# Kernel optimization log

Measured on AMD Instinct MI355X. Metric: run time of the kernel, lower is better.

## Reference

```python
import jax, jax.numpy as jnp
import numpy as np

DIM = 512
INNER = 512        # heads(8) * dim_head(64)
OUT_DIM = 256
SCALE = 64 ** -0.5  # dim_head ** -0.5
BN_EPS = 1e-5


def setup_inputs() -> dict:
    key = jax.random.key(0)
    ks = jax.random.split(key, 8)
    B, H, W = 2, 96, 320
    return {
        "left_feat": jax.random.normal(ks[0], (B, DIM, H, W), jnp.float32),
        "right_feat": jax.random.normal(ks[1], (B, DIM, H, W), jnp.float32),
        "wq": jax.random.normal(ks[2], (INNER, DIM), jnp.float32) * (DIM ** -0.5),
        "wk": jax.random.normal(ks[3], (INNER, DIM), jnp.float32) * (DIM ** -0.5),
        "wv": jax.random.normal(ks[4], (INNER, DIM), jnp.float32) * (DIM ** -0.5),
        "w1": jax.random.normal(ks[5], (OUT_DIM, INNER * 2), jnp.float32) * ((INNER * 2) ** -0.5),
        "bn_gamma": jnp.ones((OUT_DIM,), jnp.float32),
        "bn_beta": jnp.zeros((OUT_DIM,), jnp.float32),
        "bn_mean": jnp.zeros((OUT_DIM,), jnp.float32),
        "bn_var": jnp.ones((OUT_DIM,), jnp.float32),
        "w2": jax.random.normal(ks[6], (OUT_DIM, OUT_DIM), jnp.float32) * (OUT_DIM ** -0.5),
    }


def reference(left_feat, right_feat, wq, wk, wv, w1, bn_gamma, bn_beta, bn_mean, bn_var, w2):
    # conv1x1 projections, directly producing channels-last [b, h, w, c]
    q = jnp.einsum('bchw,oc->bhwo', left_feat, wq)
    k = jnp.einsum('bchw,oc->bhwo', right_feat, wk)
    v = jnp.einsum('bchw,oc->bhwo', right_feat, wv)
    # cross-attention along width, independently per (batch, row)
    dots = jnp.einsum('bhwc,bhxc->bhwx', q, k) * SCALE   # [b, h, w, w]
    attn = jax.nn.softmax(dots, axis=-1)
    out = jnp.einsum('bhwx,bhxc->bhwc', attn, v)         # [b, h, w, c]
    out = out.transpose(0, 3, 1, 2)                      # [b, c, h, w]
    new_left = jnp.concatenate([left_feat, out], axis=1)  # [b, 2*inner, h, w]
    # to_out: conv1x1 -> BN (eval mode, running stats) -> LeakyReLU(0.2) -> conv1x1
    y = jnp.einsum('bchw,oc->bohw', new_left, w1)
    inv = jax.lax.rsqrt(bn_var + BN_EPS)
    y = (y - bn_mean[None, :, None, None]) * (inv * bn_gamma)[None, :, None, None] \
        + bn_beta[None, :, None, None]
    y = jnp.where(y >= 0, y, 0.2 * y)
    return jnp.einsum('bchw,oc->bohw', y, w2)
```

## Files before the change

### kernel.cpp

```cpp
#include <hip/hip_runtime.h>

typedef __bf16 bf16x8 __attribute__((ext_vector_type(8)));
typedef float f32x4 __attribute__((ext_vector_type(4)));
typedef unsigned short u16x8 __attribute__((ext_vector_type(8)));
typedef unsigned short u16x4 __attribute__((ext_vector_type(4)));

#define MFMA16(a, b, c) __builtin_amdgcn_mfma_f32_16x16x32_bf16((a), (b), (c), 0, 0, 0)
#define GLOAD_LDS(gp, lp) __builtin_amdgcn_global_load_lds( \
    (const __attribute__((address_space(1))) void*)(uintptr_t)(const void*)(gp), \
    (__attribute__((address_space(3))) void*)(uintptr_t)(void*)(lp), 16, 0, 0)

#define NB 2
#define NC 512
#define NH 96
#define NW 320
#define PH 30720
#define NPIX 61440
#define NOUT 256

__device__ __forceinline__ unsigned short f2bf(float f) {
    union { float f; unsigned u; } v; v.f = f;
    unsigned r = v.u + 0x7fffu + ((v.u >> 16) & 1u);
    return (unsigned short)(r >> 16);
}

__global__ void k_cast(const float* __restrict__ src, unsigned short* __restrict__ dst, int n) {
    int i = blockIdx.x * 256 + threadIdx.x;
    if (i < n) dst[i] = f2bf(src[i]);
}

__global__ __launch_bounds__(256) void k_wtrans(
        const float* __restrict__ wq, const float* __restrict__ wk, const float* __restrict__ wv,
        unsigned short* __restrict__ WqT, unsigned short* __restrict__ WkT, unsigned short* __restrict__ WvT) {
    __shared__ float t[64][65];
    int z = blockIdx.z;
    const float* src = (z == 0) ? wq : (z == 1) ? wk : wv;
    unsigned short* dst = (z == 0) ? WqT : (z == 1) ? WkT : WvT;
    int i0 = blockIdx.y * 64;
    int c0 = blockIdx.x * 64;
    int tt = threadIdx.x;
    int r4 = tt >> 4, px = (tt & 15) * 4;
#pragma unroll
    for (int i = 0; i < 4; ++i) {
        int il = i * 16 + r4;
        f32x4 v = *reinterpret_cast<const f32x4*>(src + (size_t)(i0 + il) * 512 + c0 + px);
        t[il][px + 0] = v[0]; t[il][px + 1] = v[1]; t[il][px + 2] = v[2]; t[il][px + 3] = v[3];
    }
    __syncthreads();
    int cc = (tt & 7) * 8, pl0 = tt >> 3;
#pragma unroll
    for (int j = 0; j < 2; ++j) {
        int pl = j * 32 + pl0;
        u16x8 ov;
#pragma unroll
        for (int i = 0; i < 8; ++i) ov[i] = f2bf(t[cc + i][pl]);
        *reinterpret_cast<u16x8*>(dst + (size_t)(c0 + pl) * 512 + i0 + cc) = ov;
    }
}

__global__ __launch_bounds__(256) void k_transpose(
        const float* __restrict__ L, const float* __restrict__ R,
        unsigned short* __restrict__ Lcl, unsigned short* __restrict__ Rcl,
        unsigned short* __restrict__ Rbf) {
    __shared__ float t[64][65];
    int z = blockIdx.z;
    int b = z & 1, which = z >> 1;
    const float* src = which ? R : L;
    unsigned short* dst = which ? Rcl : Lcl;
    int c0 = blockIdx.y * 64;
    int p0 = blockIdx.x * 64;
    int tt = threadIdx.x;

    int cl4 = tt >> 4;
    int px = (tt & 15) * 4;
#pragma unroll
    for (int i = 0; i < 4; ++i) {
        int cl = i * 16 + cl4;
        f32x4 v = *reinterpret_cast<const f32x4*>(src + (size_t)(b * NC + c0 + cl) * PH + p0 + px);
        t[cl][px + 0] = v[0];
        t[cl][px + 1] = v[1];
        t[cl][px + 2] = v[2];
        t[cl][px + 3] = v[3];
        if (which) {
            u16x4 sv;
#pragma unroll
            for (int k = 0; k < 4; ++k) sv[k] = f2bf(v[k]);
            *reinterpret_cast<u16x4*>(Rbf + (size_t)(b * NC + c0 + cl) * PH + p0 + px) = sv;
        }
    }
    __syncthreads();

    int cc = (tt & 7) * 8;
    int pl0 = tt >> 3;
#pragma unroll
    for (int j = 0; j < 2; ++j) {
        int pl = j * 32 + pl0;
        u16x8 ov;
#pragma unroll
        for (int i = 0; i < 8; ++i) ov[i] = f2bf(t[cc + i][pl]);
        *reinterpret_cast<u16x8*>(dst + (size_t)(b * PH + p0 + pl) * NC + c0 + cc) = ov;
    }
}

template <int MODE>
__global__ __launch_bounds__(256) void k_gemm(
        const unsigned short* __restrict__ A0,
        const unsigned short* __restrict__ A1,
        const unsigned short* __restrict__ Bb,
        const unsigned short* __restrict__ Bb2,
        unsigned short* __restrict__ Dbf,
        float* __restrict__ Df32,
        const float* __restrict__ g, const float* __restrict__ be,
        const float* __restrict__ mu, const float* __restrict__ va) {
    constexpr int SA = (MODE == 4) ? NOUT : (MODE == 6) ? 1024 : NC;
    constexpr int AOFF = (MODE == 6) ? 512 : 0;
    constexpr int SB = (MODE == 3) ? 1024 : (MODE == 4) ? NOUT : NC;
    constexpr int KS = (MODE == 3) ? 32 : (MODE == 4) ? 8 : 16;
    constexpr int NTO = (MODE == 3 || MODE == 4) ? 2 : 4;
    constexpr int TOT = (MODE == 5) ? 16 : (MODE == 6) ? 8 : ((MODE == 3 || MODE == 4) ? 960 : 1920);

    __shared__ unsigned short Asm[2][128 * 32];
    __shared__ unsigned short Bsm[2][128 * 32];

    int pphys = blockIdx.x;
    int lgc = (pphys & 7) * (TOT / 8) + (pphys >> 3);
    int pixt = lgc / NTO, ot = lgc % NTO;
    const int mbase = ((MODE == 4) ? ot : pixt) * 128;
    const int nbase = ((MODE == 4) ? pixt : ot) * 128;

    const int lane = threadIdx.x & 63, w = threadIdx.x >> 6;
    const int lr = lane & 15, lg = lane >> 4;
    const int wr = w >> 1, wc = w & 1;

    auto stageA = [&](int buf, int kc) {
        const unsigned short* srcA = A0;
        int colOff = kc * 32;
        if constexpr (MODE == 3) {
            if (kc >= 16) { srcA = A1; colOff = (kc - 16) * 32; }
        }
#pragma unroll
        for (int j = 0; j < 2; ++j) {
            int cb = w * 128 + j * 64;
            int c = cb + lane;
            const unsigned short* gp = srcA + (size_t)(mbase + (c >> 2)) * SA + AOFF + colOff + (c & 3) * 8;
            GLOAD_LDS(gp, Asm[buf] + cb * 8);
        }
    };
    auto stageB = [&](int buf, int kc) {
        const unsigned short* srcB = Bb;
        int colOff = kc * 32;
        int sb = SB;
        if constexpr (MODE == 3) {
            if (kc >= 16) { srcB = Bb2; colOff = (kc - 16) * 32; sb = 512; }
        }
#pragma unroll
        for (int j = 0; j < 2; ++j) {
            int cb = w * 128 + j * 64;
            int c = cb + lane;
            const unsigned short* gp = srcB + (size_t)(nbase + (c >> 2)) * sb + colOff + (c & 3) * 8;
            GLOAD_LDS(gp, Bsm[buf] + cb * 8);
        }
    };

    f32x4 acc[4][4] = {};

    stageA(0, 0);
    stageB(0, 0);
    __syncthreads();

    for (int kc = 0; kc < KS; ++kc) {
        int cur = kc & 1;
        if (kc + 1 < KS) {
            stageA(cur ^ 1, kc + 1);
            stageB(cur ^ 1, kc + 1);
        }
        bf16x8 af[4], bfr[4];
#pragma unroll
        for (int i = 0; i < 4; ++i)
            af[i] = *reinterpret_cast<const bf16x8*>(Asm[cur] + (wr * 64 + i * 16 + lr) * 32 + lg * 8);
#pragma unroll
        for (int j = 0; j < 4; ++j)
            bfr[j] = *reinterpret_cast<const bf16x8*>(Bsm[cur] + (wc * 64 + j * 16 + lr) * 32 + lg * 8);
        __builtin_amdgcn_s_setprio(1);
#pragma unroll
        for (int i = 0; i < 4; ++i)
#pragma unroll
            for (int j = 0; j < 4; ++j)
                acc[i][j] = MFMA16(af[i], bfr[j], acc[i][j]);
        __builtin_amdgcn_s_setprio(0);
        __syncthreads();
    }

    const int lr4 = lg * 4;
    if constexpr (MODE == 0 || MODE >= 5) {
#pragma unroll
        for (int i = 0; i < 4; ++i)
#pragma unroll
            for (int j = 0; j < 4; ++j) {
                int ocol = nbase + wc * 64 + j * 16 + lr;
#pragma unroll
                for (int r = 0; r < 4; ++r) {
                    int prow = mbase + wr * 64 + i * 16 + lr4 + r;
                    Dbf[(size_t)prow * NC + ocol] = f2bf(acc[i][j][r]);
                }
            }
    } else if constexpr (MODE == 3) {
#pragma unroll
        for (int j = 0; j < 4; ++j) {
            int o = nbase + wc * 64 + j * 16 + lr;
            float sc = g[o] * rsqrtf(va[o] + 1e-5f);
            float sh = be[o] - mu[o] * sc;
#pragma unroll
            for (int i = 0; i < 4; ++i)
#pragma unroll
                for (int r = 0; r < 4; ++r) {
                    int prow = mbase + wr * 64 + i * 16 + lr4 + r;
                    float y = acc[i][j][r] * sc + sh;
                    y = (y >= 0.f) ? y : 0.2f * y;
                    Dbf[(size_t)prow * NOUT + o] = f2bf(y);
                }
        }
    } else {
#pragma unroll
        for (int j = 0; j < 4; ++j) {
            int pix = nbase + wc * 64 + j * 16 + lr;
            int b = pix / PH, ph = pix % PH;
#pragma unroll
            for (int i = 0; i < 4; ++i)
#pragma unroll
                for (int r = 0; r < 4; ++r) {
                    int o = mbase + wr * 64 + i * 16 + lr4 + r;
                    Df32[((size_t)b * NOUT + o) * PH + ph] = acc[i][j][r];
                }
        }
    }
}

__global__ __launch_bounds__(256, 2) void k_attn(
        const unsigned short* __restrict__ Q, const unsigned short* __restrict__ K,
        const unsigned short* __restrict__ Vb, unsigned short* __restrict__ O) {
    __shared__ unsigned short P[64][328];
    __shared__ unsigned short KV[32 * 512];

    int pphys = blockIdx.x;
    int l = (pphys & 7) * 120 + (pphys >> 3);
    int head = l / 5, qt = l % 5;
    int b = head / NH, hh = head % NH;
    int lane = threadIdx.x & 63, w = threadIdx.x >> 6;
    int lr = lane & 15, lg = lane >> 4;
    int rowbase = b * PH + hh * NW;
    int qrow = rowbase + qt * 64 + w * 16 + lr;

    bf16x8 qf[16];
#pragma unroll
    for (int kc = 0; kc < 16; ++kc)
        qf[kc] = *reinterpret_cast<const bf16x8*>(Q + (size_t)qrow * NC + kc * 32 + lg * 8);

    f32x4 acc[20];
#pragma unroll
    for (int xt = 0; xt < 20; ++xt) acc[xt] = f32x4{0.f, 0.f, 0.f, 0.f};

    u16x8 kreg[4];
    auto kload = [&](int t) {
#pragma unroll
        for (int j = 0; j < 4; ++j) {
            int r = w * 4 + j;
            kreg[j] = *reinterpret_cast<const u16x8*>(
                K + (size_t)(rowbase + t * 16 + r) * NC + ((lane ^ (r & 7)) * 8));
        }
    };
    auto kwrite = [&](int buf) {
#pragma unroll
        for (int j = 0; j < 4; ++j) {
            int r = w * 4 + j;
            *reinterpret_cast<u16x8*>(KV + (buf * 16 + r) * 512 + lane * 8) = kreg[j];
        }
    };

    kload(0);
    kwrite(0);
    __syncthreads();
#pragma unroll
    for (int t = 0; t < 20; ++t) {
        if (t + 1 < 20) kload(t + 1);
        int buf = t & 1;
        int rsw = lr & 7;
        __builtin_amdgcn_s_setprio(1);
#pragma unroll
        for (int kc = 0; kc < 16; ++kc) {
            bf16x8 kf = *reinterpret_cast<const bf16x8*>(
                KV + (buf * 16 + lr) * 512 + (((kc * 4 + lg) ^ rsw) * 8));
            acc[t] = MFMA16(qf[kc], kf, acc[t]);
        }
        __builtin_amdgcn_s_setprio(0);
        __syncthreads();
        if (t + 1 < 20) kwrite(buf ^ 1);
        __syncthreads();
    }

    u16x8 vreg[8];
    auto vload = [&](int s) {
#pragma unroll
        for (int j = 0; j < 8; ++j) {
            int c = (w * 8 + j) * 16 + (lane >> 2);
            int qg = (lane & 3) ^ ((lane >> 3) & 3);
            vreg[j] = *reinterpret_cast<const u16x8*>(
                Vb + (size_t)(b * NC + c) * PH + hh * NW + s * 32 + qg * 8);
        }
    };
    auto vwrite = [&]() {
#pragma unroll
        for (int j = 0; j < 8; ++j)
            *reinterpret_cast<u16x8*>(KV + (w * 8 + j) * 512 + lane * 8) = vreg[j];
    };
    vload(0);

#pragma unroll
    for (int xt = 0; xt < 20; ++xt)
#pragma unroll
        for (int r = 0; r < 4; ++r) acc[xt][r] *= 0.125f;
    float m[4] = {-1e30f, -1e30f, -1e30f, -1e30f};
#pragma unroll
    for (int xt = 0; xt < 20; ++xt)
#pragma unroll
        for (int r = 0; r < 4; ++r) m[r] = fmaxf(m[r], acc[xt][r]);
#pragma unroll
    for (int mask = 1; mask < 16; mask <<= 1)
#pragma unroll
        for (int r = 0; r < 4; ++r) m[r] = fmaxf(m[r], __shfl_xor(m[r], mask));
    float s4[4] = {0.f, 0.f, 0.f, 0.f};
#pragma unroll
    for (int xt = 0; xt < 20; ++xt)
#pragma unroll
        for (int r = 0; r < 4; ++r) {
            float e = __expf(acc[xt][r] - m[r]);
            acc[xt][r] = e;
            s4[r] += e;
        }
#pragma unroll
    for (int mask = 1; mask < 16; mask <<= 1)
#pragma unroll
        for (int r = 0; r < 4; ++r) s4[r] += __shfl_xor(s4[r], mask);
#pragma unroll
    for (int xt = 0; xt < 20; ++xt)
#pragma unroll
        for (int r = 0; r < 4; ++r)
            P[w * 16 + lg * 4 + r][xt * 16 + lr] = f2bf(acc[xt][r]);
    __syncthreads();
    vwrite();
    __syncthreads();

    f32x4 oacc[32];
#pragma unroll
    for (int ct = 0; ct < 32; ++ct) oacc[ct] = f32x4{0.f, 0.f, 0.f, 0.f};

#pragma unroll
    for (int s = 0; s < 10; ++s) {
        if (s + 1 < 10) vload(s + 1);
        bf16x8 pf = *reinterpret_cast<const bf16x8*>(&P[w * 16 + lr][s * 32 + lg * 8]);
        __builtin_amdgcn_s_setprio(1);
#pragma unroll
        for (int ct = 0; ct < 32; ++ct) {
            bf16x8 vf = *reinterpret_cast<const bf16x8*>(
                KV + ct * 512 + lr * 32 + ((lg ^ ((lr >> 1) & 3)) * 8));
            oacc[ct] = MFMA16(pf, vf, oacc[ct]);
        }
        __builtin_amdgcn_s_setprio(0);
        __syncthreads();
        if (s + 1 < 10) vwrite();
        __syncthreads();
    }

#pragma unroll
    for (int ct = 0; ct < 32; ++ct)
#pragma unroll
        for (int r = 0; r < 4; ++r) {
            int prow = rowbase + qt * 64 + w * 16 + lg * 4 + r;
            O[(size_t)prow * NC + ct * 16 + lr] = f2bf(oacc[ct][r] / s4[r]);
        }
}

extern "C" void kernel_launch(void* const* d_in, const int* in_sizes, int n_in,
                              void* d_out, int out_size, void* d_ws, size_t ws_size,
                              hipStream_t stream) {
    const float* left  = (const float*)d_in[0];
    const float* right = (const float*)d_in[1];
    const float* wq = (const float*)d_in[2];
    const float* wk = (const float*)d_in[3];
    const float* wv = (const float*)d_in[4];
    const float* w1 = (const float*)d_in[5];
    const float* bn_g = (const float*)d_in[6];
    const float* bn_b = (const float*)d_in[7];
    const float* bn_m = (const float*)d_in[8];
    const float* bn_v = (const float*)d_in[9];
    const float* w2 = (const float*)d_in[10];
    float* out = (float*)d_out;

    size_t off = 0;
    auto alloc = [&](size_t bytes) -> void* {
        void* p = (char*)d_ws + off;
        off += (bytes + 255) & ~(size_t)255;
        return p;
    };
    const size_t clb = (size_t)NPIX * NC * 2;
    unsigned short* Lcl = (unsigned short*)alloc(clb);
    unsigned short* Rcl = (unsigned short*)alloc(clb);
    unsigned short* Rbf = (unsigned short*)alloc(clb);
    unsigned short* Qb  = (unsigned short*)alloc(clb);
    unsigned short* Ub  = (unsigned short*)alloc(clb);
    unsigned short* WqT = (unsigned short*)alloc((size_t)NC * NC * 2);
    unsigned short* WkT = (unsigned short*)alloc((size_t)NC * NC * 2);
    unsigned short* WvT = (unsigned short*)alloc((size_t)NC * NC * 2);
    unsigned short* Mt  = (unsigned short*)alloc((size_t)NC * NC * 2);
    unsigned short* WX  = (unsigned short*)alloc((size_t)NOUT * NC * 2);
    unsigned short* W1b = (unsigned short*)alloc((size_t)NOUT * 1024 * 2);
    unsigned short* W2b = (unsigned short*)alloc((size_t)NOUT * NOUT * 2);
    unsigned short* Yb = Qb;

    k_cast<<<dim3((NOUT * 1024 + 255) / 256), 256, 0, stream>>>(w1, W1b, NOUT * 1024);
    k_cast<<<dim3((NOUT * NOUT + 255) / 256), 256, 0, stream>>>(w2, W2b, NOUT * NOUT);

    k_wtrans<<<dim3(8, 8, 3), 256, 0, stream>>>(wq, wk, wv, WqT, WkT, WvT);

    k_transpose<<<dim3(PH / 64, NC / 64, 4), 256, 0, stream>>>(left, right, Lcl, Rcl, Rbf);

    k_gemm<5><<<dim3(16), 256, 0, stream>>>(WkT, nullptr, WqT, nullptr, Mt, nullptr, nullptr, nullptr, nullptr, nullptr);
    k_gemm<6><<<dim3(8), 256, 0, stream>>>(W1b, nullptr, WvT, nullptr, WX, nullptr, nullptr, nullptr, nullptr, nullptr);

    k_gemm<0><<<dim3(1920), 256, 0, stream>>>(Lcl, nullptr, Mt, nullptr, Qb, nullptr, nullptr, nullptr, nullptr, nullptr);

    k_attn<<<dim3(960), 256, 0, stream>>>(Qb, Rcl, Rbf, Ub);

    k_gemm<3><<<dim3(960), 256, 0, stream>>>(Lcl, Ub, W1b, WX, Yb, nullptr, bn_g, bn_b, bn_m, bn_v);

    k_gemm<4><<<dim3(960), 256, 0, stream>>>(W2b, nullptr, Yb, nullptr, nullptr, out, nullptr, nullptr, nullptr, nullptr);
}
```

Measured before the change: 353.3 us.

## Split attention into two online-softmax halves with direct global-to-LDS staging

Restructures the attention kernel to process the 320 keys in two halves using an online softmax rescale, halving the P scratch buffer and score accumulator registers. K and V tiles are now staged with global_load_lds directly into double-buffered LDS instead of going through registers, and the V pass is split into two 256-channel halves. The smaller LDS and register footprint lets launch bounds request 3 blocks per CU to raise occupancy. The cost is extra rescale work, reloading Q per half, more barriers, and dropping the s_setprio hints.

```diff
diff --git a/kernel.cpp b/kernel.cpp
--- a/kernel.cpp
+++ b/kernel.cpp
@@ -236,11 +236,11 @@
     }
 }
 
-__global__ __launch_bounds__(256, 2) void k_attn(
+__global__ __launch_bounds__(256, 3) void k_attn(
         const unsigned short* __restrict__ Q, const unsigned short* __restrict__ K,
         const unsigned short* __restrict__ Vb, unsigned short* __restrict__ O) {
-    __shared__ unsigned short P[64][328];
-    __shared__ unsigned short KV[32 * 512];
+    __shared__ unsigned short P[64][168];
+    __shared__ unsigned short KV[2][16 * 512];
 
     int pphys = blockIdx.x;
     int l = (pphys & 7) * 120 + (pphys >> 3);
@@ -251,124 +251,120 @@
     int rowbase = b * PH + hh * NW;
     int qrow = rowbase + qt * 64 + w * 16 + lr;
 
-    bf16x8 qf[16];
-#pragma unroll
-    for (int kc = 0; kc < 16; ++kc)
-        qf[kc] = *reinterpret_cast<const bf16x8*>(Q + (size_t)qrow * NC + kc * 32 + lg * 8);
-
-    f32x4 acc[20];
-#pragma unroll
-    for (int xt = 0; xt < 20; ++xt) acc[xt] = f32x4{0.f, 0.f, 0.f, 0.f};
-
-    u16x8 kreg[4];
-    auto kload = [&](int t) {
+    auto kstage = [&](int gt, int buf) {
 #pragma unroll
         for (int j = 0; j < 4; ++j) {
             int r = w * 4 + j;
-            kreg[j] = *reinterpret_cast<const u16x8*>(
-                K + (size_t)(rowbase + t * 16 + r) * NC + ((lane ^ (r & 7)) * 8));
+            const unsigned short* gp = K + (size_t)(rowbase + gt * 16 + r) * NC + ((lane ^ (r & 7)) * 8);
+            GLOAD_LDS(gp, &KV[buf][r * 512]);
         }
     };
-    auto kwrite = [&](int buf) {
+    auto vstage = [&](int h, int s, int hc, int buf) {
 #pragma unroll
         for (int j = 0; j < 4; ++j) {
-            int r = w * 4 + j;
-            *reinterpret_cast<u16x8*>(KV + (buf * 16 + r) * 512 + lane * 8) = kreg[j];
+            int cl = (w * 4 + j) * 16 + (lane >> 2);
+            int c = hc * 256 + cl;
+            int qg = (lane & 3) ^ ((lane >> 3) & 3);
+            const unsigned short* gp = Vb + (size_t)(b * NC + c) * PH + hh * NW + h * 160 + s * 32 + qg * 8;
+            GLOAD_LDS(gp, &KV[buf][(w * 4 + j) * 512]);
         }
     };
 
-    kload(0);
-    kwrite(0);
-    __syncthreads();
-#pragma unroll
-    for (int t = 0; t < 20; ++t) {
-        if (t + 1 < 20) kload(t + 1);
-        int buf = t & 1;
-        int rsw = lr & 7;
-        __builtin_amdgcn_s_setprio(1);
-#pragma unroll
-        for (int kc = 0; kc < 16; ++kc) {
-            bf16x8 kf = *reinterpret_cast<const bf16x8*>(
-                KV + (buf * 16 + lr) * 512 + (((kc * 4 + lg) ^ rsw) * 8));
-            acc[t] = MFMA16(qf[kc], kf, acc[t]);
-        }
-        __builtin_amdgcn_s_setprio(0);
+    f32x4 oacc[32];
+#pragma unroll
+    for (int ct = 0; ct < 32; ++ct) oacc[ct] = f32x4{0.f, 0.f, 0.f, 0.f};
+    float m0[4] = {-1e30f, -1e30f, -1e30f, -1e30f};
+    float s0[4] = {0.f, 0.f, 0.f, 0.f};
+
+#pragma unroll
+    for (int h = 0; h < 2; ++h) {
+        bf16x8 qf[16];
+#pragma unroll
+        for (int kc = 0; kc < 16; ++kc)
+            qf[kc] = *reinterpret_cast<const bf16x8*>(Q + (size_t)qrow * NC + kc * 32 + lg * 8);
+
+        f32x4 acc[10];
+#pragma unroll
+        for (int xt = 0; xt < 10; ++xt) acc[xt] = f32x4{0.f, 0.f, 0.f, 0.f};
+
+        kstage(h * 10, 0);
         __syncthreads();
-        if (t + 1 < 20) kwrite(buf ^ 1);
+#pragma unroll
+        for (int t = 0; t < 10; ++t) {
+            int buf = t & 1;
+            if (t + 1 < 10) kstage(h * 10 + t + 1, buf ^ 1);
+            int rsw = lr & 7;
+#pragma unroll
+            for (int kc = 0; kc < 16; ++kc) {
+                bf16x8 kf = *reinterpret_cast<const bf16x8*>(
+                    &KV[buf][lr * 512 + (((kc * 4 + lg) ^ rsw) * 8)]);
+                acc[t] = MFMA16(qf[kc], kf, acc[t]);
+            }
+            __syncthreads();
+        }
+
+        vstage(h, 0, 0, 0);
+
+#pragma unroll
+        for (int xt = 0; xt < 10; ++xt)
+#pragma unroll
+            for (int r = 0; r < 4; ++r) acc[xt][r] *= 0.125f;
+        float mc[4] = {-1e30f, -1e30f, -1e30f, -1e30f};
+#pragma unroll
+        for (int xt = 0; xt < 10; ++xt)
+#pragma unroll
+            for (int r = 0; r < 4; ++r) mc[r] = fmaxf(mc[r], acc[xt][r]);
+#pragma unroll
+        for (int mask = 1; mask < 16; mask <<= 1)
+#pragma unroll
+            for (int r = 0; r < 4; ++r) mc[r] = fmaxf(mc[r], __shfl_xor(mc[r], mask));
+        float f0[4], sc4[4];
+#pragma unroll
+        for (int r = 0; r < 4; ++r) {
+            float nm = fmaxf(m0[r], mc[r]);
+            f0[r] = __expf(m0[r] - nm);
+            m0[r] = nm;
+            sc4[r] = 0.f;
+        }
+#pragma unroll
+        for (int xt = 0; xt < 10; ++xt)
+#pragma unroll
+            for (int r = 0; r < 4; ++r) {
+                float e = __expf(acc[xt][r] - m0[r]);
+                acc[xt][r] = e;
+                sc4[r] += e;
+            }
+#pragma unroll
+        for (int mask = 1; mask < 16; mask <<= 1)
+#pragma unroll
+            for (int r = 0; r < 4; ++r) sc4[r] += __shfl_xor(sc4[r], mask);
+#pragma unroll
+        for (int r = 0; r < 4; ++r) s0[r] = s0[r] * f0[r] + sc4[r];
+#pragma unroll
+        for (int ct = 0; ct < 32; ++ct)
+#pragma unroll
+            for (int r = 0; r < 4; ++r) oacc[ct][r] *= f0[r];
+#pragma unroll
+        for (int xt = 0; xt < 10; ++xt)
+#pragma unroll
+            for (int r = 0; r < 4; ++r)
+                P[w * 16 + lg * 4 + r][xt * 16 + lr] = f2bf(acc[xt][r]);
         __syncthreads();
-    }
-
-    u16x8 vreg[8];
-    auto vload = [&](int s) {
-#pragma unroll
-        for (int j = 0; j < 8; ++j) {
-            int c = (w * 8 + j) * 16 + (lane >> 2);
-            int qg = (lane & 3) ^ ((lane >> 3) & 3);
-            vreg[j] = *reinterpret_cast<const u16x8*>(
-                Vb + (size_t)(b * NC + c) * PH + hh * NW + s * 32 + qg * 8);
-        }
-    };
-    auto vwrite = [&]() {
-#pragma unroll
-        for (int j = 0; j < 8; ++j)
-            *reinterpret_cast<u16x8*>(KV + (w * 8 + j) * 512 + lane * 8) = vreg[j];
-    };
-    vload(0);
-
-#pragma unroll
-    for (int xt = 0; xt < 20; ++xt)
-#pragma unroll
-        for (int r = 0; r < 4; ++r) acc[xt][r] *= 0.125f;
-    float m[4] = {-1e30f, -1e30f, -1e30f, -1e30f};
-#pragma unroll
-    for (int xt = 0; xt < 20; ++xt)
-#pragma unroll
-        for (int r = 0; r < 4; ++r) m[r] = fmaxf(m[r], acc[xt][r]);
-#pragma unroll
-    for (int mask = 1; mask < 16; mask <<= 1)
-#pragma unroll
-        for (int r = 0; r < 4; ++r) m[r] = fmaxf(m[r], __shfl_xor(m[r], mask));
-    float s4[4] = {0.f, 0.f, 0.f, 0.f};
-#pragma unroll
-    for (int xt = 0; xt < 20; ++xt)
-#pragma unroll
-        for (int r = 0; r < 4; ++r) {
-            float e = __expf(acc[xt][r] - m[r]);
-            acc[xt][r] = e;
-            s4[r] += e;
-        }
-#pragma unroll
-    for (int mask = 1; mask < 16; mask <<= 1)
-#pragma unroll
-        for (int r = 0; r < 4; ++r) s4[r] += __shfl_xor(s4[r], mask);
-#pragma unroll
-    for (int xt = 0; xt < 20; ++xt)
-#pragma unroll
-        for (int r = 0; r < 4; ++r)
-            P[w * 16 + lg * 4 + r][xt * 16 + lr] = f2bf(acc[xt][r]);
-    __syncthreads();
-    vwrite();
-    __syncthreads();
-
-    f32x4 oacc[32];
-#pragma unroll
-    for (int ct = 0; ct < 32; ++ct) oacc[ct] = f32x4{0.f, 0.f, 0.f, 0.f};
-
-#pragma unroll
-    for (int s = 0; s < 10; ++s) {
-        if (s + 1 < 10) vload(s + 1);
-        bf16x8 pf = *reinterpret_cast<const bf16x8*>(&P[w * 16 + lr][s * 32 + lg * 8]);
-        __builtin_amdgcn_s_setprio(1);
-#pragma unroll
-        for (int ct = 0; ct < 32; ++ct) {
-            bf16x8 vf = *reinterpret_cast<const bf16x8*>(
-                KV + ct * 512 + lr * 32 + ((lg ^ ((lr >> 1) & 3)) * 8));
-            oacc[ct] = MFMA16(pf, vf, oacc[ct]);
-        }
-        __builtin_amdgcn_s_setprio(0);
-        __syncthreads();
-        if (s + 1 < 10) vwrite();
-        __syncthreads();
+
+#pragma unroll
+        for (int p = 0; p < 10; ++p) {
+            int buf = p & 1;
+            int s = p >> 1, hc = p & 1;
+            if (p + 1 < 10) vstage(h, (p + 1) >> 1, (p + 1) & 1, buf ^ 1);
+            bf16x8 pf = *reinterpret_cast<const bf16x8*>(&P[w * 16 + lr][s * 32 + lg * 8]);
+#pragma unroll
+            for (int cc = 0; cc < 16; ++cc) {
+                bf16x8 vf = *reinterpret_cast<const bf16x8*>(
+                    &KV[buf][cc * 512 + lr * 32 + ((lg ^ ((lr >> 1) & 3)) * 8)]);
+                oacc[hc * 16 + cc] = MFMA16(pf, vf, oacc[hc * 16 + cc]);
+            }
+            __syncthreads();
+        }
     }
 
 #pragma unroll
@@ -376,7 +372,7 @@
 #pragma unroll
         for (int r = 0; r < 4; ++r) {
             int prow = rowbase + qt * 64 + w * 16 + lg * 4 + r;
-            O[(size_t)prow * NC + ct * 16 + lr] = f2bf(oacc[ct][r] / s4[r]);
+            O[(size_t)prow * NC + ct * 16 + lr] = f2bf(oacc[ct][r] / s0[r]);
         }
 }
 
```

Result: slower. 499.5 us (+41.4%).

## Stream K via direct global-to-LDS loads, read V from global, enlarge transpose tile

Applied to the files above, without the earlier changes.

The attention kernel now stages K tiles with global_load_lds straight into shared memory instead of going through registers. V is read directly from global memory in the PV loop rather than staged in LDS. The shared buffers are merged into one smaller array so three blocks can fit per CU. The transpose kernel also processes 128 channels per block instead of 64. These changes aim to cut LDS traffic, register pressure and barrier count, at the risk of uncoalesced, higher-latency global V reads inside the MFMA loop.

```diff
diff --git a/kernel.cpp b/kernel.cpp
--- a/kernel.cpp
+++ b/kernel.cpp
@@ -62,20 +62,20 @@
         const float* __restrict__ L, const float* __restrict__ R,
         unsigned short* __restrict__ Lcl, unsigned short* __restrict__ Rcl,
         unsigned short* __restrict__ Rbf) {
-    __shared__ float t[64][65];
+    __shared__ float t[128][65];
     int z = blockIdx.z;
     int b = z & 1, which = z >> 1;
     const float* src = which ? R : L;
     unsigned short* dst = which ? Rcl : Lcl;
-    int c0 = blockIdx.y * 64;
+    int c0 = blockIdx.y * 128;
     int p0 = blockIdx.x * 64;
     int tt = threadIdx.x;
 
-    int cl4 = tt >> 4;
+    int cl16 = tt >> 4;
     int px = (tt & 15) * 4;
 #pragma unroll
-    for (int i = 0; i < 4; ++i) {
-        int cl = i * 16 + cl4;
+    for (int i = 0; i < 8; ++i) {
+        int cl = i * 16 + cl16;
         f32x4 v = *reinterpret_cast<const f32x4*>(src + (size_t)(b * NC + c0 + cl) * PH + p0 + px);
         t[cl][px + 0] = v[0];
         t[cl][px + 1] = v[1];
@@ -90,11 +90,11 @@
     }
     __syncthreads();
 
-    int cc = (tt & 7) * 8;
-    int pl0 = tt >> 3;
-#pragma unroll
-    for (int j = 0; j < 2; ++j) {
-        int pl = j * 32 + pl0;
+    int cc = (tt & 15) * 8;
+    int pl16 = tt >> 4;
+#pragma unroll
+    for (int j = 0; j < 4; ++j) {
+        int pl = j * 16 + pl16;
         u16x8 ov;
 #pragma unroll
         for (int i = 0; i < 8; ++i) ov[i] = f2bf(t[cc + i][pl]);
@@ -236,11 +236,10 @@
     }
 }
 
-__global__ __launch_bounds__(256, 2) void k_attn(
+__global__ __launch_bounds__(256, 3) void k_attn(
         const unsigned short* __restrict__ Q, const unsigned short* __restrict__ K,
         const unsigned short* __restrict__ Vb, unsigned short* __restrict__ O) {
-    __shared__ unsigned short P[64][328];
-    __shared__ unsigned short KV[32 * 512];
+    __shared__ unsigned short SH[64 * 328];
 
     int pphys = blockIdx.x;
     int l = (pphys & 7) * 120 + (pphys >> 3);
@@ -260,60 +259,31 @@
 #pragma unroll
     for (int xt = 0; xt < 20; ++xt) acc[xt] = f32x4{0.f, 0.f, 0.f, 0.f};
 
-    u16x8 kreg[4];
-    auto kload = [&](int t) {
+    auto kstage = [&](int t, int buf) {
 #pragma unroll
         for (int j = 0; j < 4; ++j) {
             int r = w * 4 + j;
-            kreg[j] = *reinterpret_cast<const u16x8*>(
-                K + (size_t)(rowbase + t * 16 + r) * NC + ((lane ^ (r & 7)) * 8));
+            const unsigned short* gp = K + (size_t)(rowbase + t * 16 + r) * NC + ((lane ^ (r & 7)) * 8);
+            GLOAD_LDS(gp, SH + buf * 8192 + r * 512);
         }
     };
-    auto kwrite = [&](int buf) {
-#pragma unroll
-        for (int j = 0; j < 4; ++j) {
-            int r = w * 4 + j;
-            *reinterpret_cast<u16x8*>(KV + (buf * 16 + r) * 512 + lane * 8) = kreg[j];
-        }
-    };
-
-    kload(0);
-    kwrite(0);
+    kstage(0, 0);
     __syncthreads();
 #pragma unroll
     for (int t = 0; t < 20; ++t) {
-        if (t + 1 < 20) kload(t + 1);
         int buf = t & 1;
+        if (t + 1 < 20) kstage(t + 1, buf ^ 1);
         int rsw = lr & 7;
         __builtin_amdgcn_s_setprio(1);
 #pragma unroll
         for (int kc = 0; kc < 16; ++kc) {
             bf16x8 kf = *reinterpret_cast<const bf16x8*>(
-                KV + (buf * 16 + lr) * 512 + (((kc * 4 + lg) ^ rsw) * 8));
+                SH + buf * 8192 + lr * 512 + (((kc * 4 + lg) ^ rsw) * 8));
             acc[t] = MFMA16(qf[kc], kf, acc[t]);
         }
         __builtin_amdgcn_s_setprio(0);
         __syncthreads();
-        if (t + 1 < 20) kwrite(buf ^ 1);
-        __syncthreads();
-    }
-
-    u16x8 vreg[8];
-    auto vload = [&](int s) {
-#pragma unroll
-        for (int j = 0; j < 8; ++j) {
-            int c = (w * 8 + j) * 16 + (lane >> 2);
-            int qg = (lane & 3) ^ ((lane >> 3) & 3);
-            vreg[j] = *reinterpret_cast<const u16x8*>(
-                Vb + (size_t)(b * NC + c) * PH + hh * NW + s * 32 + qg * 8);
-        }
-    };
-    auto vwrite = [&]() {
-#pragma unroll
-        for (int j = 0; j < 8; ++j)
-            *reinterpret_cast<u16x8*>(KV + (w * 8 + j) * 512 + lane * 8) = vreg[j];
-    };
-    vload(0);
+    }
 
 #pragma unroll
     for (int xt = 0; xt < 20; ++xt)
@@ -345,9 +315,7 @@
     for (int xt = 0; xt < 20; ++xt)
 #pragma unroll
         for (int r = 0; r < 4; ++r)
-            P[w * 16 + lg * 4 + r][xt * 16 + lr] = f2bf(acc[xt][r]);
-    __syncthreads();
-    vwrite();
+            SH[(w * 16 + lg * 4 + r) * 328 + xt * 16 + lr] = f2bf(acc[xt][r]);
     __syncthreads();
 
     f32x4 oacc[32];
@@ -356,19 +324,13 @@
 
 #pragma unroll
     for (int s = 0; s < 10; ++s) {
-        if (s + 1 < 10) vload(s + 1);
-        bf16x8 pf = *reinterpret_cast<const bf16x8*>(&P[w * 16 + lr][s * 32 + lg * 8]);
-        __builtin_amdgcn_s_setprio(1);
+        bf16x8 pf = *reinterpret_cast<const bf16x8*>(SH + (w * 16 + lr) * 328 + s * 32 + lg * 8);
 #pragma unroll
         for (int ct = 0; ct < 32; ++ct) {
             bf16x8 vf = *reinterpret_cast<const bf16x8*>(
-                KV + ct * 512 + lr * 32 + ((lg ^ ((lr >> 1) & 3)) * 8));
+                Vb + (size_t)(b * NC + ct * 16 + lr) * PH + hh * NW + s * 32 + lg * 8);
             oacc[ct] = MFMA16(pf, vf, oacc[ct]);
         }
-        __builtin_amdgcn_s_setprio(0);
-        __syncthreads();
-        if (s + 1 < 10) vwrite();
-        __syncthreads();
     }
 
 #pragma unroll
@@ -422,7 +384,7 @@
 
     k_wtrans<<<dim3(8, 8, 3), 256, 0, stream>>>(wq, wk, wv, WqT, WkT, WvT);
 
-    k_transpose<<<dim3(PH / 64, NC / 64, 4), 256, 0, stream>>>(left, right, Lcl, Rcl, Rbf);
+    k_transpose<<<dim3(PH / 64, NC / 128, 4), 256, 0, stream>>>(left, right, Lcl, Rcl, Rbf);
 
     k_gemm<5><<<dim3(16), 256, 0, stream>>>(WkT, nullptr, WqT, nullptr, Mt, nullptr, nullptr, nullptr, nullptr, nullptr);
     k_gemm<6><<<dim3(8), 256, 0, stream>>>(W1b, nullptr, WvT, nullptr, WX, nullptr, nullptr, nullptr, nullptr, nullptr);
```

Result: slower. 754.2 us (+113.5%).
